# Performance work log

Measured on AMD Instinct MI355X. Metric: run time of the kernel, lower is better.

The kernel has to match this reference:

```python
import jax, jax.numpy as jnp
import numpy as np

B, HW, FEAT = 64, 196, 2048
EMB, HID, ATT, VOCAB, T = 512, 1024, 512, 10000, 20
STEPS = T - 1  # pack_padded_sequence uses lengths - 1


def setup_inputs() -> dict:
    key = jax.random.key(0)
    ks = jax.random.split(key, 16)
    rn = lambda k, s, sc=0.02: jax.random.normal(k, s, jnp.float32) * sc
    return {
        "features": jax.random.normal(ks[0], (B, HW, FEAT), jnp.float32),
        "captions": jax.random.randint(ks[1], (B, T), 0, VOCAB),
        "lengths": jnp.full((B,), T, jnp.int32),  # uniform lengths -> constant batch per step
        "E": rn(ks[2], (VOCAB, EMB)),
        "W_feat": rn(ks[3], (EMB, FEAT)), "b_feat": jnp.zeros((EMB,), jnp.float32),
        "W1": rn(ks[4], (ATT, EMB)), "b1": jnp.zeros((ATT,), jnp.float32),
        "W2": rn(ks[5], (ATT, HID)), "b2": jnp.zeros((ATT,), jnp.float32),
        "V": rn(ks[6], (1, ATT)), "bV": jnp.zeros((1,), jnp.float32),
        "W_hi": rn(ks[7], (HID, EMB)), "b_hi": jnp.zeros((HID,), jnp.float32),
        "W_ci": rn(ks[8], (HID, EMB)), "b_ci": jnp.zeros((HID,), jnp.float32),
        "W_ih": rn(ks[9], (4 * HID, 2 * EMB)), "b_ih": jnp.zeros((4 * HID,), jnp.float32),
        "W_hh": rn(ks[10], (4 * HID, HID)), "b_hh": jnp.zeros((4 * HID,), jnp.float32),
        "W_out": rn(ks[11], (VOCAB, HID)), "b_out": jnp.zeros((VOCAB,), jnp.float32),
    }


def reference(features, captions, lengths, E, W_feat, b_feat, W1, b1, W2, b2,
              V, bV, W_hi, b_hi, W_ci, b_ci, W_ih, b_ih, W_hh, b_hh, W_out, b_out):
    # features -> embed space: [B, HW, EMB]
    f = jnp.einsum('bhc,ec->bhe', features, W_feat) + b_feat
    fmean = f.mean(axis=1)                      # [B, EMB]
    hx0 = fmean @ W_hi.T + b_hi                 # [B, HID]
    cx0 = fmean @ W_ci.T + b_ci                 # [B, HID]
    fa = jnp.einsum('bhe,ae->bha', f, W1) + b1  # W1(features), [B, HW, ATT]

    emb = E[captions]                           # [B, T, EMB]
    xs = jnp.swapaxes(emb[:, :STEPS], 0, 1)     # [STEPS, B, EMB] teacher-forced inputs

    def step(carry, x):
        hx, cx = carry
        # Bahdanau attention
        ha = hx @ W2.T + b2                             # [B, ATT]
        score = jnp.tanh(fa + ha[:, None, :])           # [B, HW, ATT]
        logits = jnp.einsum('bha,oa->bho', score, V) + bV   # [B, HW, 1]
        w = jax.nn.softmax(logits, axis=1)              # softmax over HW
        ctx = jnp.sum(w * f, axis=1)                    # [B, EMB]
        # LSTMCell (PyTorch gate order: i, f, g, o)
        inp = jnp.concatenate([x, ctx], axis=1)         # [B, 2*EMB]
        gates = inp @ W_ih.T + b_ih + hx @ W_hh.T + b_hh
        i_g, f_g, g_g, o_g = jnp.split(gates, 4, axis=1)
        cx_n = jax.nn.sigmoid(f_g) * cx + jax.nn.sigmoid(i_g) * jnp.tanh(g_g)
        hx_n = jax.nn.sigmoid(o_g) * jnp.tanh(cx_n)
        out = hx_n @ W_out.T + b_out                    # dropout = identity (eval)
        return (hx_n, cx_n), out

    _, outs = jax.lax.scan(step, (hx0, cx0), xs)        # [STEPS, B, VOCAB]
    # torch.cat(outputs) over constant per-step batch == flatten time-major
    return outs.reshape(STEPS * B, VOCAB)
```

## Files before the change

kernel.cpp:

```cpp
#include <hip/hip_runtime.h>
#include <hip/hip_bf16.h>
#include <math.h>

#define BB 64
#define HW 196
#define FEAT 2048
#define EMB 512
#define HID 1024
#define ATT 512
#define VOCAB 10000
#define TT 20
#define STEPS 19

using bfrag = __attribute__((ext_vector_type(8))) short;
using f32x4 = __attribute__((ext_vector_type(4))) float;

__device__ __forceinline__ float sigmoid_fast(float x) { return 1.0f / (1.0f + __expf(-x)); }
__device__ __forceinline__ float tanh_fast(float x) {
    float e = __expf(2.0f * x);
    return 1.0f - 2.0f / (e + 1.0f);
}
__device__ __forceinline__ ushort f2bf_rne(float f) {
    unsigned u = __float_as_uint(f);
    unsigned r = (u + 0x7FFFu + ((u >> 16) & 1u)) >> 16;
    return (ushort)r;
}
__device__ __forceinline__ float bf2f(ushort h) {
    return __uint_as_float(((unsigned)h) << 16);
}
__device__ __forceinline__ int sw_idx(int row, int g) { return row * 4 + (g ^ (row & 3)); }

__global__ __launch_bounds__(256) void k_split(const float* __restrict__ x,
                                               ushort* __restrict__ hi,
                                               ushort* __restrict__ lo, int n)
{
    int i4 = (blockIdx.x * 256 + threadIdx.x) * 4;
    if (i4 >= n) return;
    float4 v = *(const float4*)(x + i4);
    float av[4] = {v.x, v.y, v.z, v.w};
    #pragma unroll
    for (int j = 0; j < 4; ++j) {
        ushort h = f2bf_rne(av[j]);
        hi[i4 + j] = h;
        lo[i4 + j] = f2bf_rne(av[j] - bf2f(h));
    }
}

template<bool NFAST>
__global__ __launch_bounds__(256) void mfma_g(
    const float* __restrict__ A,
    const ushort* __restrict__ Bhi, const ushort* __restrict__ Blo,
    const float* __restrict__ bias, float* __restrict__ C,
    int N, int K, int ldc, int NXB, int NMB)
{
    __shared__ __align__(16) ushort sAh[256 * 8];
    __shared__ __align__(16) ushort sAl[256 * 8];
    __shared__ __align__(16) ushort sBh[512 * 8];
    __shared__ __align__(16) ushort sBl[512 * 8];

    const int tid = threadIdx.x;

    const int nwg = NXB * NMB;
    const int q = nwg >> 3, r = nwg & 7;
    const int xcd = blockIdx.x & 7, sidx = blockIdx.x >> 3;
    const int wg = (xcd < r) ? (xcd * (q + 1) + sidx)
                             : (r * (q + 1) + (xcd - r) * q + sidx);
    int im, inb;
    if (NFAST) { inb = wg % NXB; im = wg / NXB; }
    else       { im = wg % NMB; inb = wg / NMB; }
    const int m0 = im * 64;
    const int n0 = inb * 128;

    const int lane = tid & 63;
    const int w = tid >> 6;
    const int mh = (w & 1) * 32;
    const int nh = (w >> 1) * 64;
    const int g = lane >> 4, l15 = lane & 15;

    f32x4 acc[2][4] = {};

    for (int k0 = 0; k0 < K; k0 += 32) {
        __syncthreads();
        {
            int r_ = tid >> 2, g_ = tid & 3;
            const float* ap = A + (size_t)(m0 + r_) * K + k0 + g_ * 8;
            float av[8];
            *(float4*)(av)     = *(const float4*)(ap);
            *(float4*)(av + 4) = *(const float4*)(ap + 4);
            bfrag vh, vl;
            #pragma unroll
            for (int j = 0; j < 8; ++j) {
                ushort h = f2bf_rne(av[j]);
                vh[j] = (short)h;
                vl[j] = (short)f2bf_rne(av[j] - bf2f(h));
            }
            int c = sw_idx(r_, g_) * 8;
            *(bfrag*)&sAh[c] = vh;
            *(bfrag*)&sAl[c] = vl;
        }
        #pragma unroll
        for (int i = 0; i < 4; ++i) {
            int c = tid + i * 256;
            int pl = c >> 9, idx2 = c & 511;
            int r_ = idx2 >> 2, g_ = idx2 & 3;
            int brow = min(n0 + r_, N - 1);
            const ushort* src = (pl ? Blo : Bhi) + (size_t)brow * K + k0 + g_ * 8;
            int cc = sw_idx(r_, g_) * 8;
            if (pl) *(bfrag*)&sBl[cc] = *(const bfrag*)src;
            else    *(bfrag*)&sBh[cc] = *(const bfrag*)src;
        }
        __syncthreads();

        bfrag ah[2], al[2], bh[4], bl[4];
        #pragma unroll
        for (int s = 0; s < 2; ++s) {
            int c = sw_idx(mh + s * 16 + l15, g) * 8;
            ah[s] = *(const bfrag*)&sAh[c];
            al[s] = *(const bfrag*)&sAl[c];
        }
        #pragma unroll
        for (int u = 0; u < 4; ++u) {
            int c = sw_idx(nh + u * 16 + l15, g) * 8;
            bh[u] = *(const bfrag*)&sBh[c];
            bl[u] = *(const bfrag*)&sBl[c];
        }
        #pragma unroll
        for (int s = 0; s < 2; ++s)
            #pragma unroll
            for (int u = 0; u < 4; ++u) {
                acc[s][u] = __builtin_amdgcn_mfma_f32_16x16x32_bf16(ah[s], bh[u], acc[s][u], 0, 0, 0);
                acc[s][u] = __builtin_amdgcn_mfma_f32_16x16x32_bf16(ah[s], bl[u], acc[s][u], 0, 0, 0);
                acc[s][u] = __builtin_amdgcn_mfma_f32_16x16x32_bf16(al[s], bh[u], acc[s][u], 0, 0, 0);
            }
    }

    #pragma unroll
    for (int s = 0; s < 2; ++s)
        #pragma unroll
        for (int u = 0; u < 4; ++u) {
            int col = n0 + nh + u * 16 + l15;
            if (col < N) {
                float bv = bias[col];
                #pragma unroll
                for (int rr = 0; rr < 4; ++rr) {
                    int row = m0 + mh + s * 16 + g * 4 + rr;
                    C[(size_t)row * ldc + col] = acc[s][u][rr] + bv;
                }
            }
        }
}

__global__ __launch_bounds__(256) void k_fmean(const float* __restrict__ f,
                                               float* __restrict__ fmean)
{
    int b = blockIdx.x, tid = threadIdx.x;
    for (int e = tid; e < EMB; e += 256) {
        const float* fb = f + (size_t)b * HW * EMB + e;
        float s = 0.f;
        for (int h = 0; h < HW; ++h) s += fb[(size_t)h * EMB];
        fmean[b * EMB + e] = s * (1.0f / HW);
    }
}

__global__ __launch_bounds__(256) void k_init(
    const float* __restrict__ fmean,
    const float* __restrict__ W_hi, const float* __restrict__ b_hi,
    const float* __restrict__ W_ci, const float* __restrict__ b_ci,
    float* __restrict__ hx, float* __restrict__ cx)
{
    int b = blockIdx.x, tid = threadIdx.x;
    __shared__ float fm[EMB];
    for (int i = tid; i < EMB; i += 256) fm[i] = fmean[b * EMB + i];
    __syncthreads();
    for (int u = tid; u < HID; u += 256) {
        const float4* w1 = (const float4*)(W_hi + (size_t)u * EMB);
        const float4* w2 = (const float4*)(W_ci + (size_t)u * EMB);
        float a1 = b_hi[u], a2 = b_ci[u];
        for (int k = 0; k < EMB / 4; ++k) {
            float4 y1 = w1[k], y2 = w2[k];
            float x0 = fm[4*k], x1 = fm[4*k+1], x2 = fm[4*k+2], x3 = fm[4*k+3];
            a1 += x0*y1.x + x1*y1.y + x2*y1.z + x3*y1.w;
            a2 += x0*y2.x + x1*y2.y + x2*y2.z + x3*y2.w;
        }
        hx[b * HID + u] = a1;
        cx[b * HID + u] = a2;
    }
}

__global__ __launch_bounds__(128) void k_embed_split(
    const int* __restrict__ cap, const float* __restrict__ E,
    ushort* __restrict__ xs_hi, ushort* __restrict__ xs_lo)
{
    int blk = blockIdx.x;
    int t = blk / BB, b = blk % BB;
    int c = cap[b * TT + t];
    float4 v = ((const float4*)(E + (size_t)c * EMB))[threadIdx.x];
    float av[4] = {v.x, v.y, v.z, v.w};
    ushort h[4], l[4];
    #pragma unroll
    for (int j = 0; j < 4; ++j) {
        h[j] = f2bf_rne(av[j]);
        l[j] = f2bf_rne(av[j] - bf2f(h[j]));
    }
    size_t base = ((size_t)t * BB + b) * EMB + threadIdx.x * 4;
    *(ushort4*)(xs_hi + base) = make_ushort4(h[0], h[1], h[2], h[3]);
    *(ushort4*)(xs_lo + base) = make_ushort4(l[0], l[1], l[2], l[3]);
}

__global__ __launch_bounds__(256) void k_ha(
    const float* __restrict__ hx, const float* __restrict__ W2,
    const float* __restrict__ b2, float* __restrict__ ha)
{
    __shared__ __align__(16) float hx_s[8][1028];
    __shared__ float part[256];
    const int tid = threadIdx.x;
    const int a0 = (blockIdx.x >> 3) * 16;
    const int b0 = (blockIdx.x & 7) * 8;

    for (int i = tid; i < 8 * 256; i += 256) {
        int r = i >> 8, c4 = i & 255;
        *(float4*)&hx_s[r][c4 * 4] = *(const float4*)(hx + (size_t)(b0 + r) * HID + c4 * 4);
    }
    __syncthreads();

    const int a_i = tid >> 4;
    const int b_i = (tid >> 1) & 7;
    const int half = tid & 1;
    const float4* wr = (const float4*)(W2 + (size_t)(a0 + a_i) * HID + half * 512);
    const float* xr = &hx_s[b_i][half * 512];
    float s = 0.f;
    #pragma unroll 8
    for (int i = 0; i < 128; ++i) {
        float4 w = wr[i];
        float4 x = *(const float4*)(xr + i * 4);
        s += w.x*x.x + w.y*x.y + w.z*x.z + w.w*x.w;
    }
    part[tid] = s;
    __syncthreads();
    if (!half)
        ha[(size_t)(b0 + b_i) * ATT + a0 + a_i] = part[tid] + part[tid + 1] + b2[a0 + a_i];
}

__global__ __launch_bounds__(1024) void k_att(
    const float* __restrict__ f, const float* __restrict__ fa,
    const float* __restrict__ ha, const float* __restrict__ V,
    ushort* __restrict__ ctx_hi, ushort* __restrict__ ctx_lo)
{
    __shared__ __align__(16) float smem[2048];
    const int b = blockIdx.x;
    const int tid = threadIdx.x;
    const int lane = tid & 63;
    const int wid = tid >> 6;

    float* ha_s = smem;
    float* V_s  = smem + 512;
    float* w_s  = smem + 1024;
    float* red  = smem + 1280;
    float* pc   = smem + 1536;

    if (tid < ATT) { ha_s[tid] = ha[b * ATT + tid]; V_s[tid] = V[tid]; }
    __syncthreads();

    for (int h = wid; h < HW; h += 16) {
        const float4* fr = (const float4*)(fa + ((size_t)b * HW + h) * ATT);
        float s = 0.f;
        #pragma unroll
        for (int q = 0; q < 2; ++q) {
            int i4 = q * 64 + lane;
            float4 fv = fr[i4];
            float4 hv = *(const float4*)&ha_s[i4 * 4];
            float4 vv = *(const float4*)&V_s[i4 * 4];
            s += tanh_fast(fv.x + hv.x) * vv.x + tanh_fast(fv.y + hv.y) * vv.y
               + tanh_fast(fv.z + hv.z) * vv.z + tanh_fast(fv.w + hv.w) * vv.w;
        }
        #pragma unroll
        for (int off = 32; off > 0; off >>= 1) s += __shfl_down(s, off);
        if (lane == 0) w_s[h] = s;
    }
    __syncthreads();

    float v = (tid < HW) ? w_s[tid] : -INFINITY;
    if (tid < 256) red[tid] = v;
    __syncthreads();
    for (int s2 = 128; s2 > 0; s2 >>= 1) {
        if (tid < s2) red[tid] = fmaxf(red[tid], red[tid + s2]);
        __syncthreads();
    }
    float mx = red[0];
    __syncthreads();
    float e = (tid < HW) ? __expf(v - mx) : 0.f;
    if (tid < 256) red[tid] = e;
    __syncthreads();
    for (int s2 = 128; s2 > 0; s2 >>= 1) {
        if (tid < s2) red[tid] += red[tid + s2];
        __syncthreads();
    }
    float inv = 1.0f / red[0];
    if (tid < HW) w_s[tid] = e * inv;
    __syncthreads();

    {
        int e0 = tid & 511, grp = tid >> 9;
        const float* fb = f + (size_t)b * HW * EMB + e0;
        float s = 0.f;
        int h0 = grp * 98;
        for (int h = h0; h < h0 + 98; ++h)
            s = fmaf(w_s[h], fb[(size_t)h * EMB], s);
        if (grp) pc[e0] = s;
        __syncthreads();
        if (!grp) {
            float c = s + pc[e0];
            ushort ch = f2bf_rne(c);
            ctx_hi[b * EMB + e0] = ch;
            ctx_lo[b * EMB + e0] = f2bf_rne(c - bf2f(ch));
        }
    }
}

__global__ __launch_bounds__(512) void k_gates_lstm(
    const ushort* __restrict__ xsh, const ushort* __restrict__ xsl,
    const ushort* __restrict__ cth, const ushort* __restrict__ ctl,
    const ushort* __restrict__ hxh, const ushort* __restrict__ hxl,
    const ushort* __restrict__ wihh, const ushort* __restrict__ wihl,
    const ushort* __restrict__ whhh, const ushort* __restrict__ whhl,
    const float* __restrict__ b_ih, const float* __restrict__ b_hh,
    float* __restrict__ hx, float* __restrict__ cx,
    ushort* __restrict__ nxh, ushort* __restrict__ nxl,
    float* __restrict__ hx_all_t)
{
    __shared__ float sg[2][64][16];
    const int tid = threadIdx.x, bk = blockIdx.x;
    const int lane = tid & 63, wid = tid >> 6;
    const int mt = wid & 3, kh = wid >> 2;
    const int l15 = lane & 15, g = lane >> 4;
    const int arow = mt * 16 + l15;
    const int ncol = (l15 >> 2) * 1024 + bk * 4 + (l15 & 3);
    const int koff = g * 8;

    f32x4 acc0 = {}, acc1 = {};

    if (kh == 0) {
        {
            const ushort* ah = xsh + (size_t)arow * 512 + koff;
            const ushort* al = xsl + (size_t)arow * 512 + koff;
            const ushort* bh = wihh + (size_t)ncol * 1024 + koff;
            const ushort* bl = wihl + (size_t)ncol * 1024 + koff;
            #pragma unroll 4
            for (int kk = 0; kk < 16; ++kk) {
                bfrag a_h = *(const bfrag*)(ah + kk * 32);
                bfrag a_l = *(const bfrag*)(al + kk * 32);
                bfrag b_h = *(const bfrag*)(bh + kk * 32);
                bfrag b_l = *(const bfrag*)(bl + kk * 32);
                acc0 = __builtin_amdgcn_mfma_f32_16x16x32_bf16(a_h, b_h, acc0, 0, 0, 0);
                acc1 = __builtin_amdgcn_mfma_f32_16x16x32_bf16(a_h, b_l, acc1, 0, 0, 0);
                acc1 = __builtin_amdgcn_mfma_f32_16x16x32_bf16(a_l, b_h, acc1, 0, 0, 0);
            }
        }
        {
            const ushort* ah = cth + (size_t)arow * 512 + koff;
            const ushort* al = ctl + (size_t)arow * 512 + koff;
            const ushort* bh = wihh + (size_t)ncol * 1024 + 512 + koff;
            const ushort* bl = wihl + (size_t)ncol * 1024 + 512 + koff;
            #pragma unroll 4
            for (int kk = 0; kk < 16; ++kk) {
                bfrag a_h = *(const bfrag*)(ah + kk * 32);
                bfrag a_l = *(const bfrag*)(al + kk * 32);
                bfrag b_h = *(const bfrag*)(bh + kk * 32);
                bfrag b_l = *(const bfrag*)(bl + kk * 32);
                acc0 = __builtin_amdgcn_mfma_f32_16x16x32_bf16(a_h, b_h, acc0, 0, 0, 0);
                acc1 = __builtin_amdgcn_mfma_f32_16x16x32_bf16(a_h, b_l, acc1, 0, 0, 0);
                acc1 = __builtin_amdgcn_mfma_f32_16x16x32_bf16(a_l, b_h, acc1, 0, 0, 0);
            }
        }
    } else {
        const ushort* ah = hxh + (size_t)arow * 1024 + koff;
        const ushort* al = hxl + (size_t)arow * 1024 + koff;
        const ushort* bh = whhh + (size_t)ncol * 1024 + koff;
        const ushort* bl = whhl + (size_t)ncol * 1024 + koff;
        #pragma unroll 4
        for (int kk = 0; kk < 32; ++kk) {
            bfrag a_h = *(const bfrag*)(ah + kk * 32);
            bfrag a_l = *(const bfrag*)(al + kk * 32);
            bfrag b_h = *(const bfrag*)(bh + kk * 32);
            bfrag b_l = *(const bfrag*)(bl + kk * 32);
            acc0 = __builtin_amdgcn_mfma_f32_16x16x32_bf16(a_h, b_h, acc0, 0, 0, 0);
            acc1 = __builtin_amdgcn_mfma_f32_16x16x32_bf16(a_h, b_l, acc1, 0, 0, 0);
            acc1 = __builtin_amdgcn_mfma_f32_16x16x32_bf16(a_l, b_h, acc1, 0, 0, 0);
        }
    }

    #pragma unroll
    for (int rr = 0; rr < 4; ++rr)
        sg[kh][mt * 16 + g * 4 + rr][l15] = acc0[rr] + acc1[rr];
    __syncthreads();

    if (tid < 256) {
        int b = tid >> 2, uu = tid & 3;
        int u = bk * 4 + uu;
        float gi = sg[0][b][uu]      + sg[1][b][uu]      + b_ih[u]        + b_hh[u];
        float gf = sg[0][b][4 + uu]  + sg[1][b][4 + uu]  + b_ih[1024 + u] + b_hh[1024 + u];
        float gg = sg[0][b][8 + uu]  + sg[1][b][8 + uu]  + b_ih[2048 + u] + b_hh[2048 + u];
        float go = sg[0][b][12 + uu] + sg[1][b][12 + uu] + b_ih[3072 + u] + b_hh[3072 + u];
        int idx = b * 1024 + u;
        float c = sigmoid_fast(gf) * cx[idx] + sigmoid_fast(gi) * tanh_fast(gg);
        float h = sigmoid_fast(go) * tanh_fast(c);
        cx[idx] = c;
        hx[idx] = h;
        hx_all_t[idx] = h;
        ushort hh = f2bf_rne(h);
        nxh[idx] = hh;
        nxl[idx] = f2bf_rne(h - bf2f(hh));
    }
}

extern "C" void kernel_launch(void* const* d_in, const int* in_sizes, int n_in,
                              void* d_out, int out_size, void* d_ws, size_t ws_size,
                              hipStream_t stream) {
    const float* features = (const float*)d_in[0];
    const int*   captions = (const int*)d_in[1];
    const float* E      = (const float*)d_in[3];
    const float* W_feat = (const float*)d_in[4];
    const float* b_feat = (const float*)d_in[5];
    const float* W1     = (const float*)d_in[6];
    const float* b1     = (const float*)d_in[7];
    const float* W2     = (const float*)d_in[8];
    const float* b2     = (const float*)d_in[9];
    const float* V      = (const float*)d_in[10];
    const float* W_hi   = (const float*)d_in[12];
    const float* b_hi   = (const float*)d_in[13];
    const float* W_ci   = (const float*)d_in[14];
    const float* b_ci   = (const float*)d_in[15];
    const float* W_ih   = (const float*)d_in[16];
    const float* b_ih   = (const float*)d_in[17];
    const float* W_hh   = (const float*)d_in[18];
    const float* b_hh   = (const float*)d_in[19];
    const float* W_out  = (const float*)d_in[20];
    const float* b_out  = (const float*)d_in[21];
    float* out = (float*)d_out;

    float* ws = (float*)d_ws;
    float* f_buf   = ws;
    float* fa_buf  = f_buf + 6422528;
    float* fmean   = fa_buf + 6422528;
    float* hx      = fmean + 32768;
    float* cx      = hx + 65536;
    float* hx_all  = cx + 65536;
    float* ha      = hx_all + 1310720;
    ushort* p = (ushort*)(ha + 32768);
    ushort* wfeat_hi = p;            p += 1048576;
    ushort* wfeat_lo = p;            p += 1048576;
    ushort* w1_hi    = p;            p += 262144;
    ushort* w1_lo    = p;            p += 262144;
    ushort* wih_hi   = p;            p += 4194304;
    ushort* wih_lo   = p;            p += 4194304;
    ushort* whh_hi   = p;            p += 4194304;
    ushort* whh_lo   = p;            p += 4194304;
    ushort* xs_hi    = p;            p += 622592;
    ushort* xs_lo    = p;            p += 622592;
    ushort* ctx_hi   = p;            p += 32768;
    ushort* ctx_lo   = p;            p += 32768;
    ushort* hxp      = p;            p += 262144;
    ushort* wout_hi = (ushort*)f_buf;
    ushort* wout_lo = wout_hi + 10240000;

    k_split<<<1048576 / 4 / 256, 256, 0, stream>>>(W_feat, wfeat_hi, wfeat_lo, 1048576);
    k_split<<<262144 / 4 / 256, 256, 0, stream>>>(W1, w1_hi, w1_lo, 262144);
    k_split<<<4194304 / 4 / 256, 256, 0, stream>>>(W_ih, wih_hi, wih_lo, 4194304);
    k_split<<<4194304 / 4 / 256, 256, 0, stream>>>(W_hh, whh_hi, whh_lo, 4194304);
    mfma_g<true><<<784, 256, 0, stream>>>(
        features, wfeat_hi, wfeat_lo, b_feat, f_buf, 512, 2048, 512, 4, 196);
    mfma_g<true><<<784, 256, 0, stream>>>(
        f_buf, w1_hi, w1_lo, b1, fa_buf, 512, 512, 512, 4, 196);
    k_fmean<<<BB, 256, 0, stream>>>(f_buf, fmean);
    k_init<<<BB, 256, 0, stream>>>(fmean, W_hi, b_hi, W_ci, b_ci, hx, cx);
    k_split<<<65536 / 4 / 256, 256, 0, stream>>>(hx, hxp, hxp + 65536, 65536);
    k_embed_split<<<STEPS * BB, 128, 0, stream>>>(captions, E, xs_hi, xs_lo);

    for (int t = 0; t < STEPS; ++t) {
        ushort* hx_rd = hxp + (size_t)(t & 1) * 131072;
        ushort* hx_wr = hxp + (size_t)((t + 1) & 1) * 131072;
        k_ha<<<256, 256, 0, stream>>>(hx, W2, b2, ha);
        k_att<<<BB, 1024, 0, stream>>>(f_buf, fa_buf, ha, V, ctx_hi, ctx_lo);
        k_gates_lstm<<<256, 512, 0, stream>>>(
            xs_hi + (size_t)t * BB * EMB, xs_lo + (size_t)t * BB * EMB,
            ctx_hi, ctx_lo, hx_rd, hx_rd + 65536,
            wih_hi, wih_lo, whh_hi, whh_lo, b_ih, b_hh,
            hx, cx, hx_wr, hx_wr + 65536,
            hx_all + (size_t)t * BB * HID);
    }

    k_split<<<10240000 / 4 / 256, 256, 0, stream>>>(W_out, wout_hi, wout_lo, 10240000);
    mfma_g<false><<<1501, 256, 0, stream>>>(
        hx_all, wout_hi, wout_lo, b_out, out, VOCAB, HID, VOCAB, 79, 19);
}
```

Measured before the change: 1.798 ms.

## Precompute input-embedding gate projections for all steps in one batched GEMM

```diff
diff --git a/kernel.cpp b/kernel.cpp
--- a/kernel.cpp
+++ b/kernel.cpp
@@ -28,7 +28,7 @@
 __device__ __forceinline__ float bf2f(ushort h) {
     return __uint_as_float(((unsigned)h) << 16);
 }
-__device__ __forceinline__ int sw_idx(int row, int g) { return row * 4 + (g ^ (row & 3)); }
+__device__ __forceinline__ int sw_idx(int row, int g) { return row * 4 + (g ^ ((row >> 1) & 3)); }
 
 __global__ __launch_bounds__(256) void k_split(const float* __restrict__ x,
                                                ushort* __restrict__ hi,
@@ -51,7 +51,7 @@
     const float* __restrict__ A,
     const ushort* __restrict__ Bhi, const ushort* __restrict__ Blo,
     const float* __restrict__ bias, float* __restrict__ C,
-    int N, int K, int ldc, int NXB, int NMB)
+    int N, int K, int Bld, int ldc, int NXB, int NMB)
 {
     __shared__ __align__(16) ushort sAh[256 * 8];
     __shared__ __align__(16) ushort sAl[256 * 8];
@@ -104,7 +104,7 @@
             int pl = c >> 9, idx2 = c & 511;
             int r_ = idx2 >> 2, g_ = idx2 & 3;
             int brow = min(n0 + r_, N - 1);
-            const ushort* src = (pl ? Blo : Bhi) + (size_t)brow * K + k0 + g_ * 8;
+            const ushort* src = (pl ? Blo : Bhi) + (size_t)brow * Bld + k0 + g_ * 8;
             int cc = sw_idx(r_, g_) * 8;
             if (pl) *(bfrag*)&sBl[cc] = *(const bfrag*)src;
             else    *(bfrag*)&sBh[cc] = *(const bfrag*)src;
@@ -140,7 +140,7 @@
         for (int u = 0; u < 4; ++u) {
             int col = n0 + nh + u * 16 + l15;
             if (col < N) {
-                float bv = bias[col];
+                float bv = bias ? bias[col] : 0.f;
                 #pragma unroll
                 for (int rr = 0; rr < 4; ++rr) {
                     int row = m0 + mh + s * 16 + g * 4 + rr;
@@ -187,24 +187,16 @@
     }
 }
 
-__global__ __launch_bounds__(128) void k_embed_split(
-    const int* __restrict__ cap, const float* __restrict__ E,
-    ushort* __restrict__ xs_hi, ushort* __restrict__ xs_lo)
+__global__ __launch_bounds__(128) void k_embed(const int* __restrict__ cap,
+                                               const float* __restrict__ E,
+                                               float* __restrict__ xs_f)
 {
     int blk = blockIdx.x;
     int t = blk / BB, b = blk % BB;
     int c = cap[b * TT + t];
-    float4 v = ((const float4*)(E + (size_t)c * EMB))[threadIdx.x];
-    float av[4] = {v.x, v.y, v.z, v.w};
-    ushort h[4], l[4];
-    #pragma unroll
-    for (int j = 0; j < 4; ++j) {
-        h[j] = f2bf_rne(av[j]);
-        l[j] = f2bf_rne(av[j] - bf2f(h[j]));
-    }
-    size_t base = ((size_t)t * BB + b) * EMB + threadIdx.x * 4;
-    *(ushort4*)(xs_hi + base) = make_ushort4(h[0], h[1], h[2], h[3]);
-    *(ushort4*)(xs_lo + base) = make_ushort4(l[0], l[1], l[2], l[3]);
+    const float4* src = (const float4*)(E + (size_t)c * EMB);
+    float4* dst = (float4*)(xs_f + ((size_t)t * BB + b) * EMB);
+    dst[threadIdx.x] = src[threadIdx.x];
 }
 
 __global__ __launch_bounds__(256) void k_ha(
@@ -318,7 +310,7 @@
 }
 
 __global__ __launch_bounds__(512) void k_gates_lstm(
-    const ushort* __restrict__ xsh, const ushort* __restrict__ xsl,
+    const float* __restrict__ gxs_t,
     const ushort* __restrict__ cth, const ushort* __restrict__ ctl,
     const ushort* __restrict__ hxh, const ushort* __restrict__ hxl,
     const ushort* __restrict__ wihh, const ushort* __restrict__ wihl,
@@ -340,22 +332,6 @@
     f32x4 acc0 = {}, acc1 = {};
 
     if (kh == 0) {
-        {
-            const ushort* ah = xsh + (size_t)arow * 512 + koff;
-            const ushort* al = xsl + (size_t)arow * 512 + koff;
-            const ushort* bh = wihh + (size_t)ncol * 1024 + koff;
-            const ushort* bl = wihl + (size_t)ncol * 1024 + koff;
-            #pragma unroll 4
-            for (int kk = 0; kk < 16; ++kk) {
-                bfrag a_h = *(const bfrag*)(ah + kk * 32);
-                bfrag a_l = *(const bfrag*)(al + kk * 32);
-                bfrag b_h = *(const bfrag*)(bh + kk * 32);
-                bfrag b_l = *(const bfrag*)(bl + kk * 32);
-                acc0 = __builtin_amdgcn_mfma_f32_16x16x32_bf16(a_h, b_h, acc0, 0, 0, 0);
-                acc1 = __builtin_amdgcn_mfma_f32_16x16x32_bf16(a_h, b_l, acc1, 0, 0, 0);
-                acc1 = __builtin_amdgcn_mfma_f32_16x16x32_bf16(a_l, b_h, acc1, 0, 0, 0);
-            }
-        }
         {
             const ushort* ah = cth + (size_t)arow * 512 + koff;
             const ushort* al = ctl + (size_t)arow * 512 + koff;
@@ -372,13 +348,29 @@
                 acc1 = __builtin_amdgcn_mfma_f32_16x16x32_bf16(a_l, b_h, acc1, 0, 0, 0);
             }
         }
+        {
+            const ushort* ah = hxh + (size_t)arow * 1024 + koff;
+            const ushort* al = hxl + (size_t)arow * 1024 + koff;
+            const ushort* bh = whhh + (size_t)ncol * 1024 + koff;
+            const ushort* bl = whhl + (size_t)ncol * 1024 + koff;
+            #pragma unroll 4
+            for (int kk = 0; kk < 8; ++kk) {
+                bfrag a_h = *(const bfrag*)(ah + kk * 32);
+                bfrag a_l = *(const bfrag*)(al + kk * 32);
+                bfrag b_h = *(const bfrag*)(bh + kk * 32);
+                bfrag b_l = *(const bfrag*)(bl + kk * 32);
+                acc0 = __builtin_amdgcn_mfma_f32_16x16x32_bf16(a_h, b_h, acc0, 0, 0, 0);
+                acc1 = __builtin_amdgcn_mfma_f32_16x16x32_bf16(a_h, b_l, acc1, 0, 0, 0);
+                acc1 = __builtin_amdgcn_mfma_f32_16x16x32_bf16(a_l, b_h, acc1, 0, 0, 0);
+            }
+        }
     } else {
-        const ushort* ah = hxh + (size_t)arow * 1024 + koff;
-        const ushort* al = hxl + (size_t)arow * 1024 + koff;
-        const ushort* bh = whhh + (size_t)ncol * 1024 + koff;
-        const ushort* bl = whhl + (size_t)ncol * 1024 + koff;
+        const ushort* ah = hxh + (size_t)arow * 1024 + 256 + koff;
+        const ushort* al = hxl + (size_t)arow * 1024 + 256 + koff;
+        const ushort* bh = whhh + (size_t)ncol * 1024 + 256 + koff;
+        const ushort* bl = whhl + (size_t)ncol * 1024 + 256 + koff;
         #pragma unroll 4
-        for (int kk = 0; kk < 32; ++kk) {
+        for (int kk = 0; kk < 24; ++kk) {
             bfrag a_h = *(const bfrag*)(ah + kk * 32);
             bfrag a_l = *(const bfrag*)(al + kk * 32);
             bfrag b_h = *(const bfrag*)(bh + kk * 32);
@@ -397,10 +389,11 @@
     if (tid < 256) {
         int b = tid >> 2, uu = tid & 3;
         int u = bk * 4 + uu;
-        float gi = sg[0][b][uu]      + sg[1][b][uu]      + b_ih[u]        + b_hh[u];
-        float gf = sg[0][b][4 + uu]  + sg[1][b][4 + uu]  + b_ih[1024 + u] + b_hh[1024 + u];
-        float gg = sg[0][b][8 + uu]  + sg[1][b][8 + uu]  + b_ih[2048 + u] + b_hh[2048 + u];
-        float go = sg[0][b][12 + uu] + sg[1][b][12 + uu] + b_ih[3072 + u] + b_hh[3072 + u];
+        const float* gx = gxs_t + (size_t)b * 4096;
+        float gi = sg[0][b][uu]      + sg[1][b][uu]      + gx[u]        + b_ih[u]        + b_hh[u];
+        float gf = sg[0][b][4 + uu]  + sg[1][b][4 + uu]  + gx[1024 + u] + b_ih[1024 + u] + b_hh[1024 + u];
+        float gg = sg[0][b][8 + uu]  + sg[1][b][8 + uu]  + gx[2048 + u] + b_ih[2048 + u] + b_hh[2048 + u];
+        float go = sg[0][b][12 + uu] + sg[1][b][12 + uu] + gx[3072 + u] + b_ih[3072 + u] + b_hh[3072 + u];
         int idx = b * 1024 + u;
         float c = sigmoid_fast(gf) * cx[idx] + sigmoid_fast(gi) * tanh_fast(gg);
         float h = sigmoid_fast(go) * tanh_fast(c);
@@ -446,7 +439,9 @@
     float* cx      = hx + 65536;
     float* hx_all  = cx + 65536;
     float* ha      = hx_all + 1310720;
-    ushort* p = (ushort*)(ha + 32768);
+    float* xs_f    = ha + 32768;
+    float* gxs     = xs_f + 622592;
+    ushort* p = (ushort*)(gxs + 4980736);
     ushort* wfeat_hi = p;            p += 1048576;
     ushort* wfeat_lo = p;            p += 1048576;
     ushort* w1_hi    = p;            p += 262144;
@@ -455,8 +450,6 @@
     ushort* wih_lo   = p;            p += 4194304;
     ushort* whh_hi   = p;            p += 4194304;
     ushort* whh_lo   = p;            p += 4194304;
-    ushort* xs_hi    = p;            p += 622592;
-    ushort* xs_lo    = p;            p += 622592;
     ushort* ctx_hi   = p;            p += 32768;
     ushort* ctx_lo   = p;            p += 32768;
     ushort* hxp      = p;            p += 262144;
@@ -467,14 +460,16 @@
     k_split<<<262144 / 4 / 256, 256, 0, stream>>>(W1, w1_hi, w1_lo, 262144);
     k_split<<<4194304 / 4 / 256, 256, 0, stream>>>(W_ih, wih_hi, wih_lo, 4194304);
     k_split<<<4194304 / 4 / 256, 256, 0, stream>>>(W_hh, whh_hi, whh_lo, 4194304);
+    k_embed<<<STEPS * BB, 128, 0, stream>>>(captions, E, xs_f);
     mfma_g<true><<<784, 256, 0, stream>>>(
-        features, wfeat_hi, wfeat_lo, b_feat, f_buf, 512, 2048, 512, 4, 196);
+        features, wfeat_hi, wfeat_lo, b_feat, f_buf, 512, 2048, 2048, 512, 4, 196);
     mfma_g<true><<<784, 256, 0, stream>>>(
-        f_buf, w1_hi, w1_lo, b1, fa_buf, 512, 512, 512, 4, 196);
+        f_buf, w1_hi, w1_lo, b1, fa_buf, 512, 512, 512, 512, 4, 196);
+    mfma_g<false><<<608, 256, 0, stream>>>(
+        xs_f, wih_hi, wih_lo, nullptr, gxs, 4096, 512, 1024, 4096, 32, 19);
     k_fmean<<<BB, 256, 0, stream>>>(f_buf, fmean);
     k_init<<<BB, 256, 0, stream>>>(fmean, W_hi, b_hi, W_ci, b_ci, hx, cx);
     k_split<<<65536 / 4 / 256, 256, 0, stream>>>(hx, hxp, hxp + 65536, 65536);
-    k_embed_split<<<STEPS * BB, 128, 0, stream>>>(captions, E, xs_hi, xs_lo);
 
     for (int t = 0; t < STEPS; ++t) {
         ushort* hx_rd = hxp + (size_t)(t & 1) * 131072;
@@ -482,7 +477,7 @@
         k_ha<<<256, 256, 0, stream>>>(hx, W2, b2, ha);
         k_att<<<BB, 1024, 0, stream>>>(f_buf, fa_buf, ha, V, ctx_hi, ctx_lo);
         k_gates_lstm<<<256, 512, 0, stream>>>(
-            xs_hi + (size_t)t * BB * EMB, xs_lo + (size_t)t * BB * EMB,
+            gxs + (size_t)t * BB * 4096,
             ctx_hi, ctx_lo, hx_rd, hx_rd + 65536,
             wih_hi, wih_lo, whh_hi, whh_lo, b_ih, b_hh,
             hx, cx, hx_wr, hx_wr + 65536,
@@ -491,5 +486,5 @@
 
     k_split<<<10240000 / 4 / 256, 256, 0, stream>>>(W_out, wout_hi, wout_lo, 10240000);
     mfma_g<false><<<1501, 256, 0, stream>>>(
-        hx_all, wout_hi, wout_lo, b_out, out, VOCAB, HID, VOCAB, 79, 19);
-}
+        hx_all, wout_hi, wout_lo, b_out, out, VOCAB, HID, 1024, VOCAB, 79, 19);
+}
```

New measurement: 1.698 ms. 1.06x faster.
